# Optimization experiments

Hardware: AMD Instinct MI355X
Metric: run time of the kernel (lower is better)

## Reference

```python
import jax, jax.numpy as jnp
import numpy as np

N_HEAD = 12


def setup_inputs() -> dict:
    key = jax.random.key(0)
    ks = jax.random.split(key, 5)
    B, T, C = 2, 2048, 768
    x = jax.random.normal(ks[0], (B, T, C), dtype=jnp.float32)
    w_attn = jax.random.normal(ks[1], (3 * C, C), dtype=jnp.float32) * 0.02
    b_attn = jax.random.normal(ks[2], (3 * C,), dtype=jnp.float32) * 0.02
    w_proj = jax.random.normal(ks[3], (C, C), dtype=jnp.float32) * 0.02
    b_proj = jax.random.normal(ks[4], (C,), dtype=jnp.float32) * 0.02
    return {"x": x, "w_attn": w_attn, "b_attn": b_attn, "w_proj": w_proj, "b_proj": b_proj}


def reference(x, w_attn, b_attn, w_proj, b_proj):
    B, T, C = x.shape
    H = N_HEAD
    D = C // H
    # fused QKV projection (torch Linear: x @ W.T + b)
    qkv = x @ w_attn.T + b_attn                      # [B, T, 3C]
    q, k, v = jnp.split(qkv, 3, axis=-1)
    q = q.reshape(B, T, H, D).transpose(0, 2, 1, 3)  # [B, H, T, D]
    k = k.reshape(B, T, H, D).transpose(0, 2, 1, 3)
    v = v.reshape(B, T, H, D).transpose(0, 2, 1, 3)
    # NOTE: original scales by 1/sqrt(k.size(0)) == 1/sqrt(B) (batch!), reproduced faithfully
    scale = 1.0 / jnp.sqrt(jnp.asarray(B, dtype=x.dtype))
    scores = jnp.einsum("bhtd,bhsd->bhts", q, k) * scale  # [B, H, T, T]
    causal = jnp.tril(jnp.ones((T, T), dtype=bool))
    scores = jnp.where(causal[None, None], scores, jnp.asarray(-jnp.inf, dtype=x.dtype))
    attn = jax.nn.softmax(scores, axis=-1)
    # dropout layers are identity in eval mode
    out = jnp.einsum("bhts,bhsd->bhtd", attn, v)     # [B, H, T, D]
    out = out.transpose(0, 2, 1, 3).reshape(B, T, C)
    return out @ w_proj.T + b_proj
```

## Files before the change

### kernel.cpp

```cpp
#include <hip/hip_runtime.h>
#include <hip/hip_bf16.h>
#include <stdint.h>

typedef __bf16 bf16;
typedef __bf16 bf16x4 __attribute__((ext_vector_type(4)));
typedef __bf16 bf16x8 __attribute__((ext_vector_type(8)));
typedef float f32x4 __attribute__((ext_vector_type(4)));

__device__ __forceinline__ f32x4 mfma16(bf16x8 a, bf16x8 b, f32x4 c) {
    return __builtin_amdgcn_mfma_f32_16x16x32_bf16(a, b, c, 0, 0, 0);
}

__device__ __forceinline__ void gload_lds16(const void* g, void* l) {
    __builtin_amdgcn_global_load_lds((__attribute__((address_space(1))) void*)g,
                                     (__attribute__((address_space(3))) void*)l,
                                     16, 0, 0);
}

__global__ void k_cast3(const float* __restrict__ x, const float* __restrict__ wa,
                        const float* __restrict__ wp, bf16* __restrict__ xb,
                        bf16* __restrict__ wab, bf16* __restrict__ wpb) {
    const int N1 = 786432, N2 = 442368, N3 = 147456;
    int i = blockIdx.x * blockDim.x + threadIdx.x;
    int stride = gridDim.x * blockDim.x;
    for (; i < N1 + N2 + N3; i += stride) {
        const float* src; bf16* dst; int j = i;
        if (j < N1)           { src = x;  dst = xb; }
        else if (j < N1 + N2) { src = wa; dst = wab; j -= N1; }
        else                  { src = wp; dst = wpb; j -= N1 + N2; }
        float4 v = reinterpret_cast<const float4*>(src)[j];
        bf16x4 o = { (bf16)v.x, (bf16)v.y, (bf16)v.z, (bf16)v.w };
        reinterpret_cast<bf16x4*>(dst)[j] = o;
    }
}

template<bool BF16_OUT>
__global__ __launch_bounds__(256) void k_gemm_bt(
        const bf16* __restrict__ A, const bf16* __restrict__ W,
        const float* __restrict__ bias, void* __restrict__ Cout,
        int M, int N, int K) {
    __shared__ bf16 As[128 * 64];
    __shared__ bf16 Ws[128 * 64];
    const int tid = threadIdx.x;
    const int l = tid & 63, w = tid >> 6;
    const int lr = l & 15, lq = l >> 4;
    const int wm = w >> 1, wn = w & 1;
    const int bm = blockIdx.y * 128, bn = blockIdx.x * 128;

    f32x4 acc[4][4] = {};

    for (int k0 = 0; k0 < K; k0 += 64) {
        __syncthreads();
        #pragma unroll
        for (int i = 0; i < 4; ++i) {
            int c = tid + i * 256;
            int row = c >> 3, j = c & 7;
            int src8 = (j ^ (row & 7)) * 8;
            gload_lds16(A + (size_t)(bm + row) * K + k0 + src8, As + c * 8);
            gload_lds16(W + (size_t)(bn + row) * K + k0 + src8, Ws + c * 8);
        }
        __syncthreads();
        bf16x8 af[2][4], wf[2][4];
        #pragma unroll
        for (int ks = 0; ks < 2; ++ks)
            #pragma unroll
            for (int f = 0; f < 4; ++f) {
                int ra = wm * 64 + f * 16 + lr;
                int rb = wn * 64 + f * 16 + lr;
                af[ks][f] = *reinterpret_cast<const bf16x8*>(
                    As + ra * 64 + (((ks * 4 + lq) ^ (lr & 7)) * 8));
                wf[ks][f] = *reinterpret_cast<const bf16x8*>(
                    Ws + rb * 64 + (((ks * 4 + lq) ^ (lr & 7)) * 8));
            }
        #pragma unroll
        for (int ks = 0; ks < 2; ++ks)
            #pragma unroll
            for (int fm = 0; fm < 4; ++fm)
                #pragma unroll
                for (int fn = 0; fn < 4; ++fn)
                    acc[fm][fn] = mfma16(af[ks][fm], wf[ks][fn], acc[fm][fn]);
    }

    #pragma unroll
    for (int fm = 0; fm < 4; ++fm) {
        #pragma unroll
        for (int fn = 0; fn < 4; ++fn) {
            int row = bm + wm * 64 + fm * 16 + lq * 4;
            int col = bn + wn * 64 + fn * 16 + lr;
            float bv = bias[col];
            #pragma unroll
            for (int r = 0; r < 4; ++r) {
                float v = acc[fm][fn][r] + bv;
                if (BF16_OUT)
                    ((bf16*)Cout)[(size_t)(row + r) * N + col] = (bf16)v;
                else
                    ((float*)Cout)[(size_t)(row + r) * N + col] = v;
            }
        }
    }
}

#define CLOG2E 1.02014439f

__global__ __launch_bounds__(256, 4) void k_flash_attn(
        const bf16* __restrict__ qkv, bf16* __restrict__ att,
        float* __restrict__ part, int mode) {
    __shared__ bf16 Ks[3][4096];
    __shared__ bf16 Vt[2][64][64];

    const int tid = threadIdx.x;
    const int l = tid & 63, w = tid >> 6;
    const int lr = l & 15, lq = l >> 4;

    const int bid = blockIdx.x;
    int qb, h, b, jt0, jt1, slot;
    bool dopart;
    if (mode) {
        int bh = bid % 24, idx = bid / 24;
        h = bh % 12; b = bh / 12;
        if (idx < 16)      { qb = 16 + idx;  jt0 = 0;  jt1 = 16;     dopart = true;  slot = (bh * 16 + idx) * 2; }
        else if (idx < 32) { qb = 47 - idx;  jt0 = 16; jt1 = qb + 1; dopart = true;  slot = (bh * 16 + (qb - 16)) * 2 + 1; }
        else               { qb = 47 - idx;  jt0 = 0;  jt1 = qb + 1; dopart = false; slot = 0; }
    } else {
        const int s = bid >> 8, i = (bid >> 3) & 31, t7 = bid & 7;
        if (s == 0)      qb = i;
        else if (s == 2) qb = (i + 16) & 31;
        else             qb = (i < 8) ? (31 - 2 * i) : (i < 16) ? (30 - 2 * i)
                           : (i < 24) ? (62 - 2 * i) : (63 - 2 * i);
        const int hb = s * 8 + t7;
        h = hb % 12; b = hb / 12;
        jt0 = 0; jt1 = qb + 1; dopart = false; slot = 0;
    }

    const bf16* Qp = qkv + (size_t)b * 2048 * 2304 + h * 64;
    const bf16* Kp = Qp + 768;
    const bf16* Vp = Qp + 1536;

    const int qr0 = qb * 64 + w * 16;

    bf16x8 qf[2];
    #pragma unroll
    for (int ks = 0; ks < 2; ++ks)
        qf[ks] = *reinterpret_cast<const bf16x8*>(
            Qp + (size_t)(qr0 + lr) * 2304 + ks * 32 + lq * 8);

    f32x4 o[4] = {};
    float lsum = 0.f;

    auto stageK = [&](int buf, int kv0) {
        #pragma unroll
        for (int ii = 0; ii < 2; ++ii) {
            int c = tid + ii * 256;
            int row = c >> 3, j = c & 7;
            gload_lds16(Kp + (size_t)(kv0 + row) * 2304 + ((j ^ (row & 7)) * 8),
                        &Ks[buf][c * 8]);
        }
    };
    bf16x8 vv0, vv1;
    auto loadV = [&](int kv0) {
        vv0 = *reinterpret_cast<const bf16x8*>(
            Vp + (size_t)(kv0 + (tid >> 3)) * 2304 + (tid & 7) * 8);
        vv1 = *reinterpret_cast<const bf16x8*>(
            Vp + (size_t)(kv0 + 32 + (tid >> 3)) * 2304 + (tid & 7) * 8);
    };
    auto writeV = [&](int buf) {
        int kv = tid >> 3, d0 = (tid & 7) * 8, t7v = tid & 7;
        #pragma unroll
        for (int jj = 0; jj < 8; ++jj) {
            int jp = (jj + t7v) & 7;
            int d = d0 + jp, sw = jp << 3;
            Vt[buf][d][kv ^ sw]        = vv0[jp];
            Vt[buf][d][(kv + 32) ^ sw] = vv1[jp];
        }
    };

    stageK(0, jt0 * 64);
    if (jt1 > jt0 + 1) stageK(1, (jt0 + 1) * 64);
    loadV(jt0 * 64);
    asm volatile("s_waitcnt vmcnt(0)" ::: "memory");
    writeV(0);
    asm volatile("s_waitcnt lgkmcnt(0)" ::: "memory");
    __builtin_amdgcn_s_barrier();
    asm volatile("" ::: "memory");

    for (int jt = jt0; jt < jt1; ++jt) {
        const int curV = (jt - jt0) & 1;
        const int curK = (jt - jt0) % 3;
        const int kv0 = jt * 64;
        if (jt + 1 < jt1) loadV(kv0 + 64);
        if (jt + 2 < jt1) stageK((jt + 2 - jt0) % 3, kv0 + 128);

        const bool diag = (jt == qb);
        const int rsw = lr & 7;
        float p[4][4];
        __builtin_amdgcn_s_setprio(1);
        #pragma unroll
        for (int t = 0; t < 4; ++t) {
            f32x4 sacc = {0.f, 0.f, 0.f, 0.f};
            #pragma unroll
            for (int ks = 0; ks < 2; ++ks) {
                bf16x8 kf = *reinterpret_cast<const bf16x8*>(
                    &Ks[curK][(t * 16 + lr) * 64 + (((ks * 4 + lq) ^ rsw) * 8)]);
                sacc = mfma16(kf, qf[ks], sacc);
            }
            #pragma unroll
            for (int r = 0; r < 4; ++r)
                p[t][r] = __builtin_amdgcn_exp2f(sacc[r] * CLOG2E);
        }
        __builtin_amdgcn_s_setprio(0);
        if (diag) {
            #pragma unroll
            for (int t = 0; t < 4; ++t)
                #pragma unroll
                for (int r = 0; r < 4; ++r)
                    if (t * 16 + lq * 4 + r > w * 16 + lr) p[t][r] = 0.f;
        }
        {
            float s0 = (p[0][0] + p[0][1]) + (p[0][2] + p[0][3]);
            float s1 = (p[1][0] + p[1][1]) + (p[1][2] + p[1][3]);
            float s2 = (p[2][0] + p[2][1]) + (p[2][2] + p[2][3]);
            float s3 = (p[3][0] + p[3][1]) + (p[3][2] + p[3][3]);
            lsum += (s0 + s1) + (s2 + s3);
        }

        unsigned P0[4], P1[4];
        #pragma unroll
        for (int t = 0; t < 4; ++t) {
            asm("v_cvt_pk_bf16_f32 %0, %1, %2" : "=v"(P0[t]) : "v"(p[t][0]), "v"(p[t][1]));
            asm("v_cvt_pk_bf16_f32 %0, %1, %2" : "=v"(P1[t]) : "v"(p[t][2]), "v"(p[t][3]));
        }
        __builtin_amdgcn_s_setprio(1);
        #pragma unroll
        for (int ks = 0; ks < 2; ++ks) {
            unsigned a0 = P0[2 * ks], b0 = P0[2 * ks + 1];
            asm volatile("v_permlane32_swap_b32 %0, %1" : "+v"(a0), "+v"(b0));
            asm volatile("v_permlane16_swap_b32 %0, %1" : "+v"(a0), "+v"(b0));
            unsigned a1 = P1[2 * ks], b1 = P1[2 * ks + 1];
            asm volatile("v_permlane32_swap_b32 %0, %1" : "+v"(a1), "+v"(b1));
            asm volatile("v_permlane16_swap_b32 %0, %1" : "+v"(a1), "+v"(b1));
            union { unsigned u[4]; bf16x8 v8; } pk_;
            pk_.u[0] = a0; pk_.u[1] = a1; pk_.u[2] = b0; pk_.u[3] = b1;
            bf16x8 pa = pk_.v8;
            #pragma unroll
            for (int db = 0; db < 4; ++db) {
                int row = db * 16 + lr;
                bf16x8 vf = *reinterpret_cast<const bf16x8*>(
                    &Vt[curV][row][(ks * 32 + lq * 8) ^ ((row & 7) << 3)]);
                o[db] = mfma16(pa, vf, o[db]);
            }
        }
        __builtin_amdgcn_s_setprio(0);

        if (jt + 1 < jt1) writeV(curV ^ 1);
        asm volatile("s_waitcnt lgkmcnt(0)" ::: "memory");
        __builtin_amdgcn_s_barrier();
        asm volatile("" ::: "memory");
    }

    lsum += __shfl_xor(lsum, 16);
    lsum += __shfl_xor(lsum, 32);

    if (dopart) {
        float* pb = part + (size_t)slot * 4160;
        #pragma unroll
        for (int db = 0; db < 4; ++db)
            #pragma unroll
            for (int r = 0; r < 4; ++r)
                pb[(w * 16 + lq * 4 + r) * 64 + db * 16 + lr] = o[db][r];
        if (lq == 0) pb[4096 + w * 16 + lr] = lsum;
    } else {
        float inv[4];
        #pragma unroll
        for (int r = 0; r < 4; ++r)
            inv[r] = 1.0f / __shfl(lsum, lq * 4 + r);
        #pragma unroll
        for (int db = 0; db < 4; ++db)
            #pragma unroll
            for (int r = 0; r < 4; ++r) {
                float v = o[db][r] * inv[r];
                att[(size_t)(b * 2048 + qr0 + lq * 4 + r) * 768 + h * 64 + db * 16 + lr] = (bf16)v;
            }
    }
}

__global__ __launch_bounds__(256) void k_attn_reduce(
        const float* __restrict__ part, bf16* __restrict__ att) {
    int g = blockIdx.x;
    int bh = g / 16, q16 = g % 16, qb = 16 + q16;
    int h = bh % 12, b = bh / 12;
    const float* p0 = part + (size_t)((bh * 16 + q16) * 2) * 4160;
    const float* p1 = p0 + 4160;
    for (int e = threadIdx.x; e < 4096; e += 256) {
        int row = e >> 6, col = e & 63;
        float O = p0[e] + p1[e];
        float L = p0[4096 + row] + p1[4096 + row];
        att[(size_t)(b * 2048 + qb * 64 + row) * 768 + h * 64 + col] = (bf16)(O / L);
    }
}

extern "C" void kernel_launch(void* const* d_in, const int* in_sizes, int n_in,
                              void* d_out, int out_size, void* d_ws, size_t ws_size,
                              hipStream_t stream) {
    const float* x      = (const float*)d_in[0];
    const float* w_attn = (const float*)d_in[1];
    const float* b_attn = (const float*)d_in[2];
    const float* w_proj = (const float*)d_in[3];
    const float* b_proj = (const float*)d_in[4];

    char* ws = (char*)d_ws;
    bf16* xb   = (bf16*)(ws + 0);
    bf16* wab  = (bf16*)(ws + 6291456);
    bf16* wpb  = (bf16*)(ws + 9830400);
    bf16* qkv  = (bf16*)(ws + 11010048);
    bf16* att  = (bf16*)(ws + 29884416);
    float* part = (float*)(ws + 36175872);
    const unsigned long long WS_NEEDED = 36175872ull + 12779520ull;

    k_cast3<<<2048, 256, 0, stream>>>(x, w_attn, w_proj, xb, wab, wpb);

    dim3 g1(2304 / 128, 4096 / 128);
    k_gemm_bt<true><<<g1, 256, 0, stream>>>(xb, wab, b_attn, qkv, 4096, 2304, 768);

    if (ws_size >= WS_NEEDED) {
        k_flash_attn<<<1152, 256, 0, stream>>>(qkv, att, part, 1);
        k_attn_reduce<<<384, 256, 0, stream>>>(part, att);
    } else {
        k_flash_attn<<<768, 256, 0, stream>>>(qkv, att, part, 0);
    }

    dim3 g2(768 / 128, 4096 / 128);
    k_gemm_bt<false><<<g2, 256, 0, stream>>>(att, wpb, b_proj, d_out, 4096, 768, 768);
}
```

Measured before the change: 104.0 us.

## Pre-transpose V in a separate kernel and stage it via async LDS loads

Adds a small kernel that writes V transposed to [B,H,D,T] in the workspace, reusing the xb region. The attention kernel then stages V tiles with direct global-to-LDS loads in a three-deep buffer, matching how K is staged. This removes the per-iteration register load, the scattered LDS transpose writes and the lgkmcnt wait. The cost is an extra kernel launch plus a round trip of V through memory, and a larger LDS footprint that lowers the occupancy hint from 4 to 3 blocks.

```diff
diff --git a/kernel.cpp b/kernel.cpp
--- a/kernel.cpp
+++ b/kernel.cpp
@@ -100,13 +100,44 @@
     }
 }
 
+__global__ __launch_bounds__(256) void k_transV(const bf16* __restrict__ qkv,
+                                                bf16* __restrict__ vT) {
+    const int g = blockIdx.x;
+    const int bh = g >> 4, tc = g & 15;
+    const int h = bh % 12, b = bh / 12;
+    const int t0 = tc * 128;
+    __shared__ bf16 Lt[128][68];
+    const bf16* src = qkv + (size_t)(b * 2048 + t0) * 2304 + 1536 + h * 64;
+    const int tid = threadIdx.x;
+    #pragma unroll
+    for (int ii = 0; ii < 4; ++ii) {
+        int tt = ii * 32 + (tid >> 3);
+        int ch = tid & 7;
+        bf16x8 v = *reinterpret_cast<const bf16x8*>(src + (size_t)tt * 2304 + ch * 8);
+        union { bf16x8 v8; bf16x4 h4[2]; } u; u.v8 = v;
+        *reinterpret_cast<bf16x4*>(&Lt[tt][ch * 8])     = u.h4[0];
+        *reinterpret_cast<bf16x4*>(&Lt[tt][ch * 8 + 4]) = u.h4[1];
+    }
+    __syncthreads();
+    bf16* dst = vT + (size_t)bh * 64 * 2048 + t0;
+    const int d = tid >> 2;
+    #pragma unroll
+    for (int ii = 0; ii < 4; ++ii) {
+        int tch = ii * 4 + (tid & 3);
+        bf16x8 v;
+        #pragma unroll
+        for (int e = 0; e < 8; ++e) v[e] = Lt[tch * 8 + e][d];
+        *reinterpret_cast<bf16x8*>(&dst[(size_t)d * 2048 + tch * 8]) = v;
+    }
+}
+
 #define CLOG2E 1.02014439f
 
-__global__ __launch_bounds__(256, 4) void k_flash_attn(
-        const bf16* __restrict__ qkv, bf16* __restrict__ att,
-        float* __restrict__ part, int mode) {
+__global__ __launch_bounds__(256, 3) void k_flash_attn(
+        const bf16* __restrict__ qkv, const bf16* __restrict__ vT,
+        bf16* __restrict__ att, float* __restrict__ part, int mode) {
     __shared__ bf16 Ks[3][4096];
-    __shared__ bf16 Vt[2][64][64];
+    __shared__ bf16 VTs[3][4096];
 
     const int tid = threadIdx.x;
     const int l = tid & 63, w = tid >> 6;
@@ -132,9 +163,9 @@
         jt0 = 0; jt1 = qb + 1; dopart = false; slot = 0;
     }
 
-    const bf16* Qp = qkv + (size_t)b * 2048 * 2304 + h * 64;
-    const bf16* Kp = Qp + 768;
-    const bf16* Vp = Qp + 1536;
+    const bf16* Qp  = qkv + (size_t)b * 2048 * 2304 + h * 64;
+    const bf16* Kp  = Qp + 768;
+    const bf16* Vtp = vT + (size_t)(b * 12 + h) * 64 * 2048;
 
     const int qr0 = qb * 64 + w * 16;
 
@@ -156,39 +187,32 @@
                         &Ks[buf][c * 8]);
         }
     };
-    bf16x8 vv0, vv1;
-    auto loadV = [&](int kv0) {
-        vv0 = *reinterpret_cast<const bf16x8*>(
-            Vp + (size_t)(kv0 + (tid >> 3)) * 2304 + (tid & 7) * 8);
-        vv1 = *reinterpret_cast<const bf16x8*>(
-            Vp + (size_t)(kv0 + 32 + (tid >> 3)) * 2304 + (tid & 7) * 8);
+    auto stageV = [&](int buf, int kv0) {
+        #pragma unroll
+        for (int ii = 0; ii < 2; ++ii) {
+            int c = tid + ii * 256;
+            int row = c >> 3, j = c & 7;
+            gload_lds16(Vtp + (size_t)row * 2048 + kv0 + ((j ^ (row & 7)) * 8),
+                        &VTs[buf][c * 8]);
+        }
     };
-    auto writeV = [&](int buf) {
-        int kv = tid >> 3, d0 = (tid & 7) * 8, t7v = tid & 7;
-        #pragma unroll
-        for (int jj = 0; jj < 8; ++jj) {
-            int jp = (jj + t7v) & 7;
-            int d = d0 + jp, sw = jp << 3;
-            Vt[buf][d][kv ^ sw]        = vv0[jp];
-            Vt[buf][d][(kv + 32) ^ sw] = vv1[jp];
-        }
-    };
 
     stageK(0, jt0 * 64);
-    if (jt1 > jt0 + 1) stageK(1, (jt0 + 1) * 64);
-    loadV(jt0 * 64);
-    asm volatile("s_waitcnt vmcnt(0)" ::: "memory");
-    writeV(0);
-    asm volatile("s_waitcnt lgkmcnt(0)" ::: "memory");
+    stageV(0, jt0 * 64);
+    const bool two = (jt1 > jt0 + 1);
+    if (two) { stageK(1, jt0 * 64 + 64); stageV(1, jt0 * 64 + 64); }
+    if (two) asm volatile("s_waitcnt vmcnt(4)" ::: "memory");
+    else     asm volatile("s_waitcnt vmcnt(0)" ::: "memory");
     __builtin_amdgcn_s_barrier();
     asm volatile("" ::: "memory");
 
     for (int jt = jt0; jt < jt1; ++jt) {
-        const int curV = (jt - jt0) & 1;
-        const int curK = (jt - jt0) % 3;
+        const int cur = (jt - jt0) % 3;
         const int kv0 = jt * 64;
-        if (jt + 1 < jt1) loadV(kv0 + 64);
-        if (jt + 2 < jt1) stageK((jt + 2 - jt0) % 3, kv0 + 128);
+        if (jt + 2 < jt1) {
+            stageK((jt + 2 - jt0) % 3, kv0 + 128);
+            stageV((jt + 2 - jt0) % 3, kv0 + 128);
+        }
 
         const bool diag = (jt == qb);
         const int rsw = lr & 7;
@@ -200,7 +224,7 @@
             #pragma unroll
             for (int ks = 0; ks < 2; ++ks) {
                 bf16x8 kf = *reinterpret_cast<const bf16x8*>(
-                    &Ks[curK][(t * 16 + lr) * 64 + (((ks * 4 + lq) ^ rsw) * 8)]);
+                    &Ks[cur][(t * 16 + lr) * 64 + (((ks * 4 + lq) ^ rsw) * 8)]);
                 sacc = mfma16(kf, qf[ks], sacc);
             }
             #pragma unroll
@@ -229,7 +253,6 @@
             asm("v_cvt_pk_bf16_f32 %0, %1, %2" : "=v"(P0[t]) : "v"(p[t][0]), "v"(p[t][1]));
             asm("v_cvt_pk_bf16_f32 %0, %1, %2" : "=v"(P1[t]) : "v"(p[t][2]), "v"(p[t][3]));
         }
-        __builtin_amdgcn_s_setprio(1);
         #pragma unroll
         for (int ks = 0; ks < 2; ++ks) {
             unsigned a0 = P0[2 * ks], b0 = P0[2 * ks + 1];
@@ -241,18 +264,20 @@
             union { unsigned u[4]; bf16x8 v8; } pk_;
             pk_.u[0] = a0; pk_.u[1] = a1; pk_.u[2] = b0; pk_.u[3] = b1;
             bf16x8 pa = pk_.v8;
+            __builtin_amdgcn_s_setprio(1);
             #pragma unroll
             for (int db = 0; db < 4; ++db) {
-                int row = db * 16 + lr;
                 bf16x8 vf = *reinterpret_cast<const bf16x8*>(
-                    &Vt[curV][row][(ks * 32 + lq * 8) ^ ((row & 7) << 3)]);
+                    &VTs[cur][(db * 16 + lr) * 64 + (((ks * 4 + lq) ^ rsw) * 8)]);
                 o[db] = mfma16(pa, vf, o[db]);
             }
-        }
-        __builtin_amdgcn_s_setprio(0);
-
-        if (jt + 1 < jt1) writeV(curV ^ 1);
-        asm volatile("s_waitcnt lgkmcnt(0)" ::: "memory");
+            __builtin_amdgcn_s_setprio(0);
+        }
+
+        if (jt + 1 < jt1) {
+            if (jt + 2 < jt1) asm volatile("s_waitcnt vmcnt(4)" ::: "memory");
+            else              asm volatile("s_waitcnt vmcnt(0)" ::: "memory");
+        }
         __builtin_amdgcn_s_barrier();
         asm volatile("" ::: "memory");
     }
@@ -309,6 +334,7 @@
 
     char* ws = (char*)d_ws;
     bf16* xb   = (bf16*)(ws + 0);
+    bf16* vT   = (bf16*)(ws + 0);
     bf16* wab  = (bf16*)(ws + 6291456);
     bf16* wpb  = (bf16*)(ws + 9830400);
     bf16* qkv  = (bf16*)(ws + 11010048);
@@ -321,11 +347,13 @@
     dim3 g1(2304 / 128, 4096 / 128);
     k_gemm_bt<true><<<g1, 256, 0, stream>>>(xb, wab, b_attn, qkv, 4096, 2304, 768);
 
+    k_transV<<<384, 256, 0, stream>>>(qkv, vT);
+
     if (ws_size >= WS_NEEDED) {
-        k_flash_attn<<<1152, 256, 0, stream>>>(qkv, att, part, 1);
+        k_flash_attn<<<1152, 256, 0, stream>>>(qkv, vT, att, part, 1);
         k_attn_reduce<<<384, 256, 0, stream>>>(part, att);
     } else {
-        k_flash_attn<<<768, 256, 0, stream>>>(qkv, att, part, 0);
+        k_flash_attn<<<768, 256, 0, stream>>>(qkv, vT, att, part, 0);
     }
 
     dim3 g2(768 / 128, 4096 / 128);
```

Measured after the change: 91.53 us. 1.14x faster.
